# Optimization experiments

Measured on AMD Instinct MI355X. Metric: run time of the kernel, lower is better.

Reference implementation:

```python
import jax, jax.numpy as jnp
import numpy as np

INPUT_DIM = 10              # number of binary covariates in x
N = 2_000_000               # batch size
C = 2 ** (INPUT_DIM + 1)    # 2048 (t, x) combinations, one Linear(1,1) each


def setup_inputs() -> dict:
    key = jax.random.key(0)
    kx, kt, ky, kw, kb = jax.random.split(key, 5)
    x = jax.random.randint(kx, (N, INPUT_DIM), 0, 2).astype(jnp.float32)  # binary covariates
    t = jax.random.randint(kt, (N, 1), 0, 2).astype(jnp.float32)          # binary treatment
    y = jax.random.normal(ky, (N, 1), dtype=jnp.float32)                  # outcome
    # Per-combination Linear(1,1): weight w[i] and bias b[i] for q_z_dummies[i]
    w = jax.random.normal(kw, (C,), dtype=jnp.float32) * 0.5
    b = jax.random.normal(kb, (C,), dtype=jnp.float32) * 0.5
    return {"x": x, "t": t, "y": y, "w": w, "b": b}


def reference(x, t, y, w, b):
    # The torch loop sums (w_i*y + b_i) * [exact match of (t, x) with combination i].
    # Exactly one combination matches per row, so this equals a gather at the
    # combination index. itertools.product([0,1], repeat=d+1) orders bits
    # (t, x_0, ..., x_{d-1}) with the FIRST bit most significant.
    powers = (2 ** jnp.arange(INPUT_DIM - 1, -1, -1)).astype(x.dtype)      # [d]
    idx = (t[:, 0] * (2 ** INPUT_DIM) + x @ powers).astype(jnp.int32)      # [N]
    z_logits = y * w[idx][:, None] + b[idx][:, None]                       # [N, 1]
    # Original returns (z_mu=0, z_var=0, z_logits) in binary mode; z_logits is
    # the only tensor output.
    return z_logits
```

## Files before the change

### kernel.cpp

```cpp
#include <hip/hip_runtime.h>
#include <hip/hip_bf16.h>


#define INPUT_DIM 10

__global__ __launch_bounds__(256) void enc_kernel(
    const float* __restrict__ x,
    const float* __restrict__ t,
    const float* __restrict__ y,
    const float* __restrict__ w,
    const float* __restrict__ b,
    float* __restrict__ out,
    int n)
{
    int i = blockIdx.x * blockDim.x + threadIdx.x;
    if (i >= n) return;

    const float2* xr = (const float2*)(x + (size_t)i * INPUT_DIM);
    float2 a0 = xr[0];
    float2 a1 = xr[1];
    float2 a2 = xr[2];
    float2 a3 = xr[3];
    float2 a4 = xr[4];

    int idx = ((int)t[i]) << 10;
    idx |= ((int)a0.x << 9) | ((int)a0.y << 8)
         | ((int)a1.x << 7) | ((int)a1.y << 6)
         | ((int)a2.x << 5) | ((int)a2.y << 4)
         | ((int)a3.x << 3) | ((int)a3.y << 2)
         | ((int)a4.x << 1) | ((int)a4.y);

    out[i] = fmaf(y[i], w[idx], b[idx]);
}

extern "C" void kernel_launch(void* const* d_in, const int* in_sizes, int n_in,
                              void* d_out, int out_size, void* d_ws, size_t ws_size,
                              hipStream_t stream) {
    const float* x = (const float*)d_in[0];
    const float* t = (const float*)d_in[1];
    const float* y = (const float*)d_in[2];
    const float* w = (const float*)d_in[3];
    const float* b = (const float*)d_in[4];
    float* out = (float*)d_out;

    int n = out_size;
    int block = 256;
    int grid = (n + block - 1) / block;
    enc_kernel<<<grid, block, 0, stream>>>(x, t, y, w, b, out, n);
}
```

Baseline: 132.5 us.

## Stage x tiles into LDS via async global_load_lds with persistent waves

```diff
diff --git a/kernel.cpp b/kernel.cpp
--- a/kernel.cpp
+++ b/kernel.cpp
@@ -2,34 +2,102 @@
 #include <hip/hip_bf16.h>
 
 
-#define INPUT_DIM 10
+#define D          10
+#define C_TAB      2048
+#define TILE_ROWS  128
+#define BLOCKS     1024
+#define WPB        4
 
-__global__ __launch_bounds__(256) void enc_kernel(
+__device__ __forceinline__ void async_load16(const void* g, void* l) {
+    __builtin_amdgcn_global_load_lds(
+        (const __attribute__((address_space(1))) void*)g,
+        (__attribute__((address_space(3))) void*)l, 16, 0, 0);
+}
+
+__device__ __forceinline__ int make_idx(const float* row, float tt) {
+    const float2* p = (const float2*)row;
+    float2 a0 = p[0], a1 = p[1], a2 = p[2], a3 = p[3], a4 = p[4];
+    float v = a0.x;
+    v = fmaf(v, 2.f, a0.y);
+    v = fmaf(v, 2.f, a1.x);
+    v = fmaf(v, 2.f, a1.y);
+    v = fmaf(v, 2.f, a2.x);
+    v = fmaf(v, 2.f, a2.y);
+    v = fmaf(v, 2.f, a3.x);
+    v = fmaf(v, 2.f, a3.y);
+    v = fmaf(v, 2.f, a4.x);
+    v = fmaf(v, 2.f, a4.y);
+    v = fmaf(tt, 1024.f, v);
+    return (int)v;
+}
+
+__global__ __launch_bounds__(256, 4) void enc_kernel(
     const float* __restrict__ x,
     const float* __restrict__ t,
     const float* __restrict__ y,
     const float* __restrict__ w,
     const float* __restrict__ b,
     float* __restrict__ out,
-    int n)
+    int nTiles, int nTotalWaves)
 {
-    int i = blockIdx.x * blockDim.x + threadIdx.x;
+    __shared__ float lw[C_TAB];
+    __shared__ float lb[C_TAB];
+    __shared__ float xs[WPB][TILE_ROWS * D];
+
+    const int tid = threadIdx.x;
+
+    {
+        const float4* w4 = (const float4*)w;
+        const float4* b4 = (const float4*)b;
+        float4* lw4 = (float4*)lw;
+        float4* lb4 = (float4*)lb;
+        lw4[tid]       = w4[tid];
+        lw4[tid + 256] = w4[tid + 256];
+        lb4[tid]       = b4[tid];
+        lb4[tid + 256] = b4[tid + 256];
+    }
+    __syncthreads();
+
+    const int wave = tid >> 6;
+    const int lane = tid & 63;
+    float* xw = xs[wave];
+
+    for (int tile = blockIdx.x * WPB + wave; tile < nTiles; tile += nTotalWaves) {
+        const char* gbase = (const char*)x + (size_t)tile * (TILE_ROWS * D * 4);
+        #pragma unroll
+        for (int k = 0; k < 5; ++k) {
+            async_load16(gbase + k * 1024 + lane * 16, (char*)xw + k * 1024);
+        }
+
+        const int r0 = tile * TILE_ROWS + lane;
+        const int r1 = r0 + 64;
+        float t0 = t[r0], t1 = t[r1];
+        float y0 = y[r0], y1 = y[r1];
+
+        __builtin_amdgcn_s_waitcnt(0);
+        __asm__ volatile("" ::: "memory");
+
+        const int i0 = make_idx(&xw[lane * D], t0);
+        const int i1 = make_idx(&xw[(lane + 64) * D], t1);
+
+        out[r0] = fmaf(y0, lw[i0], lb[i0]);
+        out[r1] = fmaf(y1, lw[i1], lb[i1]);
+    }
+}
+
+__global__ __launch_bounds__(256) void enc_tail(
+    const float* __restrict__ x, const float* __restrict__ t,
+    const float* __restrict__ y, const float* __restrict__ w,
+    const float* __restrict__ b, float* __restrict__ out,
+    int start, int n)
+{
+    int i = start + blockIdx.x * blockDim.x + threadIdx.x;
     if (i >= n) return;
-
-    const float2* xr = (const float2*)(x + (size_t)i * INPUT_DIM);
-    float2 a0 = xr[0];
-    float2 a1 = xr[1];
-    float2 a2 = xr[2];
-    float2 a3 = xr[3];
-    float2 a4 = xr[4];
-
-    int idx = ((int)t[i]) << 10;
-    idx |= ((int)a0.x << 9) | ((int)a0.y << 8)
-         | ((int)a1.x << 7) | ((int)a1.y << 6)
-         | ((int)a2.x << 5) | ((int)a2.y << 4)
-         | ((int)a3.x << 3) | ((int)a3.y << 2)
-         | ((int)a4.x << 1) | ((int)a4.y);
-
+    const float* r = x + (size_t)i * D;
+    float v = r[0];
+    #pragma unroll
+    for (int j = 1; j < D; ++j) v = fmaf(v, 2.f, r[j]);
+    int idx = (int)fmaf(t[i], 1024.f, v);
     out[i] = fmaf(y[i], w[idx], b[idx]);
 }
 
@@ -43,8 +111,14 @@
     const float* b = (const float*)d_in[4];
     float* out = (float*)d_out;
 
-    int n = out_size;
-    int block = 256;
-    int grid = (n + block - 1) / block;
-    enc_kernel<<<grid, block, 0, stream>>>(x, t, y, w, b, out, n);
+    const int n = out_size;
+    const int nTiles = n / TILE_ROWS;
+    const int rem = n - nTiles * TILE_ROWS;
+
+    enc_kernel<<<BLOCKS, 256, 0, stream>>>(x, t, y, w, b, out,
+                                           nTiles, BLOCKS * WPB);
+    if (rem > 0) {
+        enc_tail<<<(rem + 255) / 256, 256, 0, stream>>>(
+            x, t, y, w, b, out, nTiles * TILE_ROWS, n);
+    }
 }
```

New measurement: 134.9 us. No clear change (+1.7%).
